# Kernel optimization log

Measured on AMD Instinct MI355X. Metric: run time of the kernel, lower is better.

## Reference

```python
import jax, jax.numpy as jnp
import numpy as np

jax.config.update("jax_enable_x64", True)

N = 3
NX = (N ** 2) ** 3          # 729 decision vars (flattened 9x9x9 one-hot board)
M2 = 128                    # dense inequality rows (G2)
QPEN = 0.1                  # Qpenalty -> Q = QPEN * I
NITER = 10                  # fixed interior-point iterations
SIGMA = 0.1                 # centering parameter
B = 16                      # batch of puzzles


def setup_inputs() -> dict:
    key = jax.random.key(0)
    k1, k2 = jax.random.split(key)
    puzzles = jax.random.uniform(k1, (B, 9, 9, 9), dtype=jnp.float32)
    G2 = jax.random.uniform(k2, (M2, NX), minval=-1.0, maxval=1.0, dtype=jnp.float32)
    z2 = jnp.zeros((NX,), jnp.float32)
    s2 = jnp.ones((M2,), jnp.float32)
    return {"puzzles": puzzles, "G2": G2, "z2": z2, "s2": s2}


def _qp_solve(p, G2, h):
    """Solve min 0.5 z'Qz + p'z  s.t. [-I; G2] z <= h for a batch of p.

    Primal-dual interior-point method, fixed NITER steps, exploiting the
    block structure G = [-I; G2]:  G' D G = diag(d1) + G2' D2 G2.
    p: (B, NX) float64. Returns z: (B, NX).
    """
    Bn, nx = p.shape
    G = jnp.concatenate([-jnp.eye(nx, dtype=p.dtype), G2], axis=0)  # (m, nx)
    m = G.shape[0]
    eye = jnp.eye(nx, dtype=p.dtype)

    z0 = jnp.zeros((Bn, nx), p.dtype)
    s0 = jnp.ones((Bn, m), p.dtype)
    lam0 = jnp.ones((Bn, m), p.dtype)

    def maxstep(x, dx):
        # largest alpha<=1 keeping x + alpha*dx > 0 (fraction-to-boundary 0.99)
        ratio = jnp.where(dx < 0, -x / jnp.where(dx < 0, dx, -1.0), jnp.inf)
        return jnp.minimum(1.0, 0.99 * jnp.min(ratio, axis=1))

    def step(carry, _):
        z, s, lam = carry
        Gz = z @ G.T                                   # (B, m)
        rd = QPEN * z + p + lam @ G                    # dual residual (B, nx)
        rp = Gz + s - h                                # primal residual (B, m)
        mu = jnp.mean(s * lam, axis=1, keepdims=True)  # (B, 1)
        d = lam / s                                    # (B, m)
        v = SIGMA * mu / s - lam + d * rp              # (B, m)
        rhs = -(rd + v @ G)                            # (B, nx)
        # K = Q + G' D G = diag(QPEN + d1) + G2' D2 G2  (block-sparse structure)
        K = jnp.einsum('mi,bm,mj->bij', G2, d[:, nx:], G2)
        K = K + eye[None] * (QPEN + d[:, :nx])[:, :, None]
        dz = jnp.linalg.solve(K, rhs[..., None])[..., 0]
        Gdz = dz @ G.T
        ds = -rp - Gdz
        dlam = v + d * Gdz
        alpha = jnp.minimum(maxstep(s, ds), maxstep(lam, dlam))[:, None]
        return (z + alpha * dz, s + alpha * ds, lam + alpha * dlam), None

    (z, _, _), _ = jax.lax.scan(step, (z0, s0, lam0), None, length=NITER)
    return z


def reference(puzzles, G2, z2, s2):
    Bn = puzzles.shape[0]
    G2d = G2.astype(jnp.float64)
    z2d = z2.astype(jnp.float64)
    s2d = s2.astype(jnp.float64)
    p = -puzzles.reshape(Bn, -1).astype(jnp.float64)     # (B, NX)
    h2 = G2d @ z2d + s2d                                 # (M2,)
    h = jnp.concatenate([jnp.zeros(NX, jnp.float64), h2])
    z = _qp_solve(p, G2d, h)
    return z.astype(jnp.float32).reshape(puzzles.shape)
```

## Files before the change

### kernel.cpp

```cpp
#include <hip/hip_runtime.h>
#include <math.h>

#define NXQ 729
#define M2Q 128
#define MQ  857
#define BQ  16
#define QPEN_ 0.1
#define SIGMA_ 0.1

typedef double d4 __attribute__((ext_vector_type(4)));

constexpr int OFF_P    = 0;
constexpr int OFF_H2   = OFF_P + BQ*NXQ;
constexpr int OFF_Q2   = OFF_H2 + M2Q;
constexpr int OFF_TP   = OFF_Q2 + BQ*M2Q;
constexpr int ST_Z    = 0;
constexpr int ST_S    = 729;
constexpr int ST_LAM  = 1586;
constexpr int ST_RP   = 2443;
constexpr int ST_V    = 3300;
constexpr int ST_AINV = 4157;
constexpr int ST_Y    = 4886;
constexpr int ST_GZ   = 5615;
constexpr int STB     = 5743;
constexpr int OFF_ST  = OFF_TP + 12*BQ*M2Q;
constexpr int OFF_SG  = OFF_ST + 2*BQ*STB;

constexpr int L_SL   = 0;
constexpr int L_US   = 16512;
constexpr int L_INVD = 16640;
constexpr int L_RED2 = 16768;
constexpr int SH_FUSED = (16768 + 544) * 8;
constexpr int D_DZ   = 0;
constexpr int D_RED  = 736;
constexpr int D_SC   = 744;
constexpr int D_Q2   = 752;
constexpr int D_YL   = 880;
constexpr int D_SN   = 944;
constexpr int D_LN   = 1801;
constexpr int D_PART = 2658;
constexpr int D_AINV = 12672;
constexpr int AR_W   = 3168;
constexpr int SH_PS  = 12672 * 8;

__device__ __constant__ int TRI_R[10] = {0,1,1,2,2,2,3,3,3,3};
__device__ __constant__ int TRI_C[10] = {0,0,1,0,1,2,0,1,2,3};
__device__ __constant__ int TRL_R[28] = {0,1,1,2,2,2,3,3,3,3,4,4,4,4,4,5,5,5,5,5,5,6,6,6,6,6,6,6};
__device__ __constant__ int TRL_C[28] = {0,0,1,0,1,2,0,1,2,3,0,1,2,3,4,0,1,2,3,4,5,0,1,2,3,4,5,6};

__device__ __forceinline__ double wred_sum(double v) {
#pragma unroll
  for (int off = 32; off > 0; off >>= 1) v += __shfl_down(v, off, 64);
  return v;
}
__device__ __forceinline__ double wred_min(double v) {
#pragma unroll
  for (int off = 32; off > 0; off >>= 1) v = fmin(v, __shfl_down(v, off, 64));
  return v;
}
__device__ __forceinline__ double rsqrt64(double x) {
  double r = (double)rsqrtf((float)x);
  r = r * (1.5 - 0.5 * x * r * r);
  r = r * (1.5 - 0.5 * x * r * r);
  return r;
}

__global__ __launch_bounds__(512)
void init_kernel(const float* __restrict__ puzzles, const float* __restrict__ G2,
                 const float* __restrict__ z2in, const float* __restrict__ s2in,
                 double* __restrict__ ws) {
  const int blk = blockIdx.x;
  const int tid = threadIdx.x, wave = tid >> 6, lane = tid & 63;
  __shared__ double sm[32];
  if (blk < BQ) {
    const int bb = blk;
    double* st = ws + OFF_ST + bb * STB;
    for (int i = tid; i < NXQ; i += 512) {
      ws[OFF_P + bb * NXQ + i] = -(double)puzzles[bb * NXQ + i];
      st[ST_Z + i] = 0.0;
      st[ST_AINV + i] = 1.0 / (QPEN_ + 1.0);
      st[ST_RP + i] = 1.0;
      st[ST_V + i] = SIGMA_;
    }
    for (int i = tid; i < MQ; i += 512) { st[ST_S + i] = 1.0; st[ST_LAM + i] = 1.0; }
    if (tid < M2Q) st[ST_GZ + tid] = 0.0;
  } else {
    const int r = blk - 16;
    double acc = 0.0;
    for (int kx = tid; kx < NXQ; kx += 512)
      acc += (double)G2[r * NXQ + kx] * (double)z2in[kx];
    acc = wred_sum(acc);
    if (lane == 0) sm[wave] = acc;
    __syncthreads();
    if (tid == 0) {
      double t = 0.0;
#pragma unroll
      for (int w = 0; w < 8; ++w) t += sm[w];
      const double h2r = t + (double)s2in[r];
      ws[OFF_H2 + r] = h2r;
      sm[16] = h2r;
    }
    __syncthreads();
    if (tid < BQ) {
      double* st = ws + OFF_ST + tid * STB;
      const double rp2 = 1.0 - sm[16];
      st[ST_RP + NXQ + r] = rp2;
      st[ST_V  + NXQ + r] = rp2 - 0.9;
      ws[OFF_Q2 + tid * M2Q + r] = rp2 + 0.1;
    }
  }
}

__device__ __forceinline__ void sbuild_core(const float* __restrict__ G2,
                                            const double* __restrict__ ainv,
                                            double* __restrict__ arena,
                                            double* __restrict__ Sgb, const int tile) {
  const int tid = threadIdx.x, wave = tid >> 6, lane = tid & 63;
  const int R0 = TRI_R[tile] * 32, C0 = TRI_C[tile] * 32;
  double* As = arena + wave * AR_W;
  double* Bs = As + 1584;
  const int k0w = wave * 183;
  const int kend = min(k0w + 183, NXQ);
  const int rg4 = (lane >> 3) * 4, cg4 = (lane & 7) * 4;
  const int kk16 = lane & 15, rsub = lane >> 4;
  double acc[4][4];
#pragma unroll
  for (int i = 0; i < 4; ++i)
#pragma unroll
    for (int j = 0; j < 4; ++j) acc[i][j] = 0.0;
  float pa[24], pb[24];
  if (wave < 4) {
#pragma unroll
    for (int it = 0; it < 24; ++it) {
      const int kk = (it >> 3) * 16 + kk16;
      const int rr = (it & 7) * 4 + rsub;
      const int k = k0w + kk;
      const int kc = (k < kend) ? k : (kend - 1);
      pa[it] = G2[(R0 + rr) * NXQ + kc];
      pb[it] = G2[(C0 + rr) * NXQ + kc];
    }
  }
  for (int ch = 0; ch < 4; ++ch) {
    __syncthreads();
    if (wave < 4) {
#pragma unroll
      for (int it = 0; it < 24; ++it) {
        const int kk = (it >> 3) * 16 + kk16;
        const int rr = (it & 7) * 4 + rsub;
        const int k = k0w + ch * 48 + kk;
        const bool ok = (k < kend);
        const double aik = ok ? ainv[k] : 0.0;
        const double av = ok ? (double)pa[it] * aik : 0.0;
        const double bv = ok ? (double)pb[it] : 0.0;
        As[kk * 33 + rr] = av;
        Bs[kk * 33 + rr] = bv;
      }
      if (ch < 3) {
#pragma unroll
        for (int it = 0; it < 24; ++it) {
          const int kk = (it >> 3) * 16 + kk16;
          const int rr = (it & 7) * 4 + rsub;
          const int k = k0w + (ch + 1) * 48 + kk;
          const int kc = (k < kend) ? k : (kend - 1);
          pa[it] = G2[(R0 + rr) * NXQ + kc];
          pb[it] = G2[(C0 + rr) * NXQ + kc];
        }
      }
    }
    __syncthreads();
    if (wave < 4) {
#pragma unroll 8
      for (int q = 0; q < 48; ++q) {
        const double a0 = As[q*33 + rg4 + 0], a1 = As[q*33 + rg4 + 1],
                     a2 = As[q*33 + rg4 + 2], a3 = As[q*33 + rg4 + 3];
        const double b0 = Bs[q*33 + cg4 + 0], b1 = Bs[q*33 + cg4 + 1],
                     b2 = Bs[q*33 + cg4 + 2], b3 = Bs[q*33 + cg4 + 3];
        acc[0][0] += a0*b0; acc[0][1] += a0*b1; acc[0][2] += a0*b2; acc[0][3] += a0*b3;
        acc[1][0] += a1*b0; acc[1][1] += a1*b1; acc[1][2] += a1*b2; acc[1][3] += a1*b3;
        acc[2][0] += a2*b0; acc[2][1] += a2*b1; acc[2][2] += a2*b2; acc[2][3] += a2*b3;
        acc[3][0] += a3*b0; acc[3][1] += a3*b1; acc[3][2] += a3*b2; acc[3][3] += a3*b3;
      }
    }
  }
  __syncthreads();
  if (wave < 4) {
#pragma unroll
    for (int i = 0; i < 4; ++i)
#pragma unroll
      for (int j = 0; j < 4; ++j)
        As[(rg4 + i) * 33 + cg4 + j] = acc[i][j];
  }
  __syncthreads();
  for (int idx = tid; idx < 1024; idx += 512) {
    const int r = idx >> 5, c = idx & 31;
    const int o = r * 33 + c;
    const double v = arena[o] + arena[AR_W + o] + arena[2*AR_W + o] + arena[3*AR_W + o];
    Sgb[tile * 1024 + idx] = v;
  }
}

__global__ __launch_bounds__(512)
void ps_kernel(const float* __restrict__ G2, double* __restrict__ ws) {
  const int b = blockIdx.x, tile = blockIdx.y;
  const int tid = threadIdx.x, lane = tid & 63;
  extern __shared__ double sm[];
  double* st = ws + OFF_ST + b * STB;
  {
    double* uvec = sm;
    double* part = sm + 128;
    double* yl   = sm + 640;
    const int c0 = tile * 64;
    if (tid < M2Q) uvec[tid] = ws[OFF_Q2 + b * M2Q + tid];
    __syncthreads();
    const int kk = tid & 63, rq = tid >> 6;
    const int k = c0 + kk;
    const int kg = (k < NXQ) ? k : (NXQ - 1);
    {
      const float* gp = G2 + (rq * 16) * NXQ + kg;
      double acc = 0.0;
#pragma unroll
      for (int j = 0; j < 16; ++j) acc = fma((double)gp[j * NXQ], uvec[rq * 16 + j], acc);
      part[rq * 64 + kk] = acc;
    }
    __syncthreads();
    if (tid < 64) {
      const int k2 = c0 + tid;
      double y = 0.0;
      if (k2 < NXQ) {
        double w = 0.0;
#pragma unroll
        for (int q = 0; q < 8; ++q) w += part[q * 64 + tid];
        const double rhsk = -(QPEN_ * st[ST_Z + k2] + ws[OFF_P + b * NXQ + k2]
                              - st[ST_LAM + k2] - st[ST_V + k2] + w);
        y = st[ST_AINV + k2] * rhsk;
        st[ST_Y + k2] = y;
      }
      yl[tid] = y;
    }
    __syncthreads();
    {
      const double yv = yl[lane];
      double pp[16];
#pragma unroll
      for (int jr = 0; jr < 16; ++jr)
        pp[jr] = (double)G2[((tid >> 6) * 16 + jr) * NXQ + kg] * yv;
#pragma unroll
      for (int st2 = 0; st2 < 4; ++st2) {
        const int m = 32 >> st2, half = 8 >> st2;
        const bool hi = (lane & m) != 0;
#pragma unroll
        for (int r = 0; r < 8; ++r) {
          if (r < half) {
            const double send = hi ? pp[r] : pp[r + half];
            const double recv = __shfl_xor(send, m, 64);
            pp[r] = (hi ? pp[r + half] : pp[r]) + recv;
          }
        }
      }
      double tot = pp[0];
      tot += __shfl_xor(tot, 2, 64);
      tot += __shfl_xor(tot, 1, 64);
      if ((lane & 3) == 0)
        ws[OFF_TP + (tile * BQ + b) * M2Q + (tid >> 6) * 16 + ((lane >> 2) & 15)] = tot;
    }
    __syncthreads();
  }
  if (tile < 10)
    sbuild_core(G2, st + ST_AINV, sm, ws + OFF_SG + b * 10240, tile);
}

__global__ __launch_bounds__(512, 1)
void dps_kernel(const float* __restrict__ G2, double* __restrict__ ws,
                float* __restrict__ out, const int ph, const int last) {
  const int b = blockIdx.x, chunk = blockIdx.y;
  const int tid = threadIdx.x, wave = tid >> 6, lane = tid & 63;
  extern __shared__ double sm[];
  double (*Sl)[129] = (double(*)[129])(sm + L_SL);
  double* us   = sm + L_US;
  double* invd = sm + L_INVD;
  double* red2 = sm + L_RED2;
  const double* R = ws + OFF_ST + ph * BQ * STB + b * STB;
  double*       W = ws + OFF_ST + (1 - ph) * BQ * STB + b * STB;
  double* Sgb  = ws + OFF_SG + b * 10240;
  const int c0 = chunk * 64;

#pragma unroll
  for (int t = 0; t < 10; ++t) {
    const int R0 = TRI_R[t] * 32, C0 = TRI_C[t] * 32;
    for (int e = tid; e < 1024; e += 512) {
      const int r = e >> 5, c = e & 31;
      Sl[R0 + r][C0 + c] = Sgb[t * 1024 + e];
    }
  }
  if (tid < M2Q) {
    double t = 0.0;
#pragma unroll
    for (int c = 0; c < 12; ++c) t += ws[OFF_TP + (c * BQ + b) * M2Q + tid];
    us[tid] = t;
  }
  __syncthreads();
  if (tid < M2Q) Sl[tid][tid] += R[ST_S + NXQ + tid] / R[ST_LAM + NXQ + tid];
  __syncthreads();

  int rowm[4], colm[4];
  {
    const int rc = lane & 15, kq = lane >> 4;
    const double avr = (kq == 0) ? (double)rc : 0.0;
    const double bv1 = (kq == 0) ? 1.0 : 0.0;
    const double av1 = (kq == 0) ? 1.0 : 0.0;
    const double bvc = (kq == 0) ? (double)rc : 0.0;
    d4 zero = {0.0, 0.0, 0.0, 0.0};
    d4 dr = __builtin_amdgcn_mfma_f64_16x16x4f64(avr, bv1, zero, 0, 0, 0);
    d4 dc = __builtin_amdgcn_mfma_f64_16x16x4f64(av1, bvc, zero, 0, 0, 0);
#pragma unroll
    for (int e = 0; e < 4; ++e) { rowm[e] = (int)dr[e]; colm[e] = (int)dc[e]; }
  }
  const int rc16 = lane & 15, kq4 = lane >> 4;

  auto panel16 = [&](const int K0) {
    const int r = lane;
    double a[16];
#pragma unroll
    for (int c = 0; c < 16; ++c) a[c] = Sl[K0 + r][K0 + c];
#pragma unroll
    for (int c = 0; c < 16; ++c) {
      const double dcc = __shfl(a[c], c, 64);
      const double rs = rsqrt64(dcc);
      a[c] *= rs;
      if (lane == c) invd[K0 + c] = rs;
#pragma unroll
      for (int k2 = c + 1; k2 < 16; ++k2) {
        const double lkc = __shfl(a[c], k2, 64);
        a[k2] = fma(-a[c], lkc, a[k2]);
      }
    }
#pragma unroll
    for (int c = 0; c < 16; ++c) Sl[K0 + r][K0 + c] = a[c];
  };

  auto tile_upd = [&](const int K0, const int i0, const int j0) {
    d4 tacc;
#pragma unroll
    for (int e = 0; e < 4; ++e) tacc[e] = Sl[i0 + rowm[e]][j0 + colm[e]];
#pragma unroll
    for (int m = 0; m < 4; ++m) {
      const double av = -Sl[i0 + rc16][K0 + 4 * m + kq4];
      const double bv =  Sl[j0 + rc16][K0 + 4 * m + kq4];
      tacc = __builtin_amdgcn_mfma_f64_16x16x4f64(av, bv, tacc, 0, 0, 0);
    }
#pragma unroll
    for (int e = 0; e < 4; ++e) Sl[i0 + rowm[e]][j0 + colm[e]] = tacc[e];
  };

  if (wave == 0 && lane < 16) panel16(0);
  __syncthreads();

  for (int kb = 0; kb < 8; ++kb) {
    const int K0 = kb * 16, J0 = K0 + 16, T = 128 - J0;
    if (tid <= T) {
      const bool isU = (tid == T);
      double l[16];
      if (isU) {
#pragma unroll
        for (int c = 0; c < 16; ++c) l[c] = us[K0 + c];
      } else {
#pragma unroll
        for (int c = 0; c < 16; ++c) l[c] = Sl[J0 + tid][K0 + c];
      }
#pragma unroll
      for (int c = 0; c < 16; ++c) {
        const double lc = l[c] * invd[K0 + c];
        l[c] = lc;
#pragma unroll
        for (int k2 = c + 1; k2 < 16; ++k2)
          l[k2] = fma(-lc, Sl[K0 + k2][K0 + c], l[k2]);
      }
      if (isU) {
#pragma unroll
        for (int c = 0; c < 16; ++c) us[K0 + c] = l[c];
      } else {
#pragma unroll
        for (int c = 0; c < 16; ++c) Sl[J0 + tid][K0 + c] = l[c];
      }
    }
    __syncthreads();

    if (kb < 7) {
      if (tid < T) {
        double acc = 0.0;
#pragma unroll
        for (int c = 0; c < 16; ++c) acc = fma(Sl[J0 + tid][K0 + c], us[K0 + c], acc);
        us[J0 + tid] -= acc;
      }
      if (wave == 7) tile_upd(K0, J0, J0);
      __syncthreads();
      const int Tb = 7 - kb;
      const int nt = (Tb * (Tb + 1)) >> 1;
      if (wave == 0) {
        if (lane < 16) panel16(J0);
      } else {
        for (int idx = wave; idx < nt; idx += 7)
          tile_upd(K0, J0 + TRL_R[idx] * 16, J0 + TRL_C[idx] * 16);
      }
      __syncthreads();
    }
  }

  for (int kb = 7; kb >= 0; --kb) {
    const int K0 = kb * 16;
    if (kb < 7) {
      const int c = tid & 15, ch = tid >> 4;
      double part = 0.0;
      for (int k = K0 + 16 + ch; k < 128; k += 32) part = fma(Sl[k][K0 + c], us[k], part);
      red2[ch * 17 + c] = part;
    }
    __syncthreads();
    if (wave == 0 && lane < 16) {
      const int j = lane;
      double x = us[K0 + j];
      if (kb < 7) {
        double acc = 0.0;
#pragma unroll
        for (int q = 0; q < 32; ++q) acc += red2[q * 17 + j];
        x -= acc;
      }
      double colv[16];
#pragma unroll
      for (int c = 0; c < 16; ++c) colv[c] = Sl[K0 + c][K0 + j];
      const double iv = invd[K0 + j];
#pragma unroll
      for (int cc = 0; cc < 16; ++cc) {
        const int c = 15 - cc;
        const double xiv = x * iv;
        const double uc = __shfl(xiv, c, 64);
        if (j == c) x = xiv;
        else if (j < c) x = fma(-colv[c], uc, x);
      }
      us[K0 + j] = x;
    }
    __syncthreads();
  }
  if (tid < M2Q) invd[tid] = (R[ST_S + NXQ + tid] / R[ST_LAM + NXQ + tid]) * us[tid];
  __syncthreads();
  double* g2b = invd;

  double* dzl   = sm + D_DZ;
  double* red   = sm + D_RED;
  double* sc    = sm + D_SC;
  double* ainvn = sm + D_AINV;
  double* q2l   = sm + D_Q2;
  double* yl    = sm + D_YL;
  double* snew  = sm + D_SN;
  double* lnew  = sm + D_LN;
  double* part  = sm + D_PART;

  for (int k = tid; k < NXQ; k += 512) {
    double acc = 0.0;
    const float* gp = G2 + k;
#pragma unroll 16
    for (int r = 0; r < M2Q; ++r) acc = fma((double)gp[r * NXQ], us[r], acc);
    dzl[k] = R[ST_Y + k] - R[ST_AINV + k] * acc;
  }
  __syncthreads();

  double lmin = 1e300;
  for (int i = tid; i < MQ; i += 512) {
    const double si = R[ST_S + i], li = R[ST_LAM + i], di = li / si;
    double dsi, dlami;
    if (i < NXQ) {
      const double dz = dzl[i];
      dsi = dz - R[ST_RP + i];
      dlami = R[ST_V + i] - di * dz;
    } else {
      const double g = g2b[i - NXQ];
      dsi = -R[ST_RP + i] - g;
      dlami = R[ST_V + i] + di * g;
    }
    snew[i] = dsi; lnew[i] = dlami;
    if (dsi < 0.0)   lmin = fmin(lmin, -si / dsi);
    if (dlami < 0.0) lmin = fmin(lmin, -li / dlami);
  }
  lmin = wred_min(lmin);
  if (lane == 0) red[wave] = lmin;
  __syncthreads();
  if (tid == 0) {
    double m = red[0];
#pragma unroll
    for (int w = 1; w < 8; ++w) m = fmin(m, red[w]);
    sc[0] = fmin(1.0, 0.99 * m);
  }
  __syncthreads();
  const double alpha = sc[0];

  if (last) {
    const int k2 = c0 + (tid & 63);
    if (tid < 64 && k2 < NXQ)
      out[b * NXQ + k2] = (float)(R[ST_Z + k2] + alpha * dzl[k2]);
    return;
  }

  double musum = 0.0;
  for (int i = tid; i < MQ; i += 512) {
    const double si = R[ST_S + i], li = R[ST_LAM + i];
    const double sn = si + alpha * snew[i], ln = li + alpha * lnew[i];
    snew[i] = sn; lnew[i] = ln;
    musum += sn * ln;
  }
  musum = wred_sum(musum);
  if (lane == 0) red[wave] = musum;
  __syncthreads();
  if (tid == 0) {
    double t = 0.0;
#pragma unroll
    for (int w = 0; w < 8; ++w) t += red[w];
    sc[1] = SIGMA_ * (t / (double)MQ);
  }
  __syncthreads();
  const double smu = sc[1];

  for (int i = tid; i < MQ; i += 512) {
    const double sn = snew[i], ln = lnew[i], di = ln / sn;
    if (i < NXQ) {
      const double zn = R[ST_Z + i] + alpha * dzl[i];
      const double rpn = sn - zn;
      const double vn = smu / sn - ln + di * rpn;
      const double an = 1.0 / (QPEN_ + di);
      ainvn[i] = an;
      if ((i >> 6) == chunk) {
        W[ST_Z + i] = zn; W[ST_S + i] = sn; W[ST_LAM + i] = ln;
        W[ST_RP + i] = rpn; W[ST_V + i] = vn; W[ST_AINV + i] = an;
      }
    } else {
      const int m = i - NXQ;
      const double gzn = R[ST_GZ + m] + alpha * g2b[m];
      const double rpn = gzn + sn - ws[OFF_H2 + m];
      const double vn = smu / sn - ln + di * rpn;
      q2l[m] = ln + vn;
      if (chunk == 0) {
        W[ST_S + i] = sn; W[ST_LAM + i] = ln;
        W[ST_RP + i] = rpn; W[ST_V + i] = vn; W[ST_GZ + m] = gzn;
      }
    }
  }
  __syncthreads();

  {
    const int kk = tid & 63, rq = tid >> 6;
    const int k = c0 + kk;
    const int kg = (k < NXQ) ? k : (NXQ - 1);
    {
      const float* gp = G2 + (rq * 16) * NXQ + kg;
      double acc = 0.0;
#pragma unroll
      for (int j = 0; j < 16; ++j) acc = fma((double)gp[j * NXQ], q2l[rq * 16 + j], acc);
      part[rq * 64 + kk] = acc;
    }
    __syncthreads();
    if (tid < 64) {
      const int k2 = c0 + tid;
      double y = 0.0;
      if (k2 < NXQ) {
        double w = 0.0;
#pragma unroll
        for (int q = 0; q < 8; ++q) w += part[q * 64 + tid];
        const double sn = snew[k2], ln = lnew[k2], di = ln / sn;
        const double zn = R[ST_Z + k2] + alpha * dzl[k2];
        const double rpn = sn - zn;
        const double vn = smu / sn - ln + di * rpn;
        const double rhsk = -(QPEN_ * zn + ws[OFF_P + b * NXQ + k2] - ln - vn + w);
        y = ainvn[k2] * rhsk;
        W[ST_Y + k2] = y;
      }
      yl[tid] = y;
    }
    __syncthreads();
    {
      const double yv = yl[lane];
      double pp[16];
#pragma unroll
      for (int jr = 0; jr < 16; ++jr)
        pp[jr] = (double)G2[((tid >> 6) * 16 + jr) * NXQ + kg] * yv;
#pragma unroll
      for (int st2 = 0; st2 < 4; ++st2) {
        const int m = 32 >> st2, half = 8 >> st2;
        const bool hi = (lane & m) != 0;
#pragma unroll
        for (int r = 0; r < 8; ++r) {
          if (r < half) {
            const double send = hi ? pp[r] : pp[r + half];
            const double recv = __shfl_xor(send, m, 64);
            pp[r] = (hi ? pp[r + half] : pp[r]) + recv;
          }
        }
      }
      double tot = pp[0];
      tot += __shfl_xor(tot, 2, 64);
      tot += __shfl_xor(tot, 1, 64);
      if ((lane & 3) == 0)
        ws[OFF_TP + (chunk * BQ + b) * M2Q + (tid >> 6) * 16 + ((lane >> 2) & 15)] = tot;
    }
    __syncthreads();
  }

  if (chunk < 10)
    sbuild_core(G2, ainvn, sm, Sgb, chunk);
}

extern "C" void kernel_launch(void* const* d_in, const int* in_sizes, int n_in,
                              void* d_out, int out_size, void* d_ws, size_t ws_size,
                              hipStream_t stream) {
  const float* puzzles = (const float*)d_in[0];
  const float* G2      = (const float*)d_in[1];
  const float* z2      = (const float*)d_in[2];
  const float* s2      = (const float*)d_in[3];
  float* out = (float*)d_out;
  double* ws = (double*)d_ws;

  (void)hipFuncSetAttribute(reinterpret_cast<const void*>(&dps_kernel),
                            hipFuncAttributeMaxDynamicSharedMemorySize, SH_FUSED);
  (void)hipFuncSetAttribute(reinterpret_cast<const void*>(&ps_kernel),
                            hipFuncAttributeMaxDynamicSharedMemorySize, SH_PS);

  init_kernel<<<dim3(16 + M2Q), dim3(512), 0, stream>>>(puzzles, G2, z2, s2, ws);
  ps_kernel<<<dim3(BQ, 12), dim3(512), SH_PS, stream>>>(G2, ws);
  for (int it = 0; it < 10; ++it) {
    const int ph = it & 1;
    dps_kernel<<<dim3(BQ, 12), dim3(512), SH_FUSED, stream>>>(G2, ws, out, ph, (it == 9) ? 1 : 0);
  }
}
```

Baseline: 970.5 us.

## Split S-build tiles into K-halves computed with FP64 MFMA across more blocks

The G2'DG2 tile build now uses FP64 MFMA 16x16x4 instructions instead of scalar FMA outer products. Each tile's K range is split into two halves written as separate partial buffers, which the consumer sums on load. The grid grows from 12 to 16 blocks per batch so more CUs share the S-build work. The dz computation is also fused with the step-length ratio loop, removing one barrier. The cost is a larger workspace, extra partial-sum reads, and more blocks per launch.

```diff
diff --git a/kernel.cpp b/kernel.cpp
--- a/kernel.cpp
+++ b/kernel.cpp
@@ -24,6 +24,7 @@
 constexpr int ST_GZ   = 5615;
 constexpr int STB     = 5743;
 constexpr int OFF_ST  = OFF_TP + 12*BQ*M2Q;
+constexpr int SGB_B   = 20480;
 constexpr int OFF_SG  = OFF_ST + 2*BQ*STB;
 
 constexpr int L_SL   = 0;
@@ -65,6 +66,20 @@
   return r;
 }
 
+__device__ __forceinline__ void mfma_cdmap(int* rowm, int* colm) {
+  const int lane = threadIdx.x & 63;
+  const int rc = lane & 15, kq = lane >> 4;
+  const double avr = (kq == 0) ? (double)rc : 0.0;
+  const double bv1 = (kq == 0) ? 1.0 : 0.0;
+  const double av1 = (kq == 0) ? 1.0 : 0.0;
+  const double bvc = (kq == 0) ? (double)rc : 0.0;
+  d4 zero = {0.0, 0.0, 0.0, 0.0};
+  d4 dr = __builtin_amdgcn_mfma_f64_16x16x4f64(avr, bv1, zero, 0, 0, 0);
+  d4 dc = __builtin_amdgcn_mfma_f64_16x16x4f64(av1, bvc, zero, 0, 0, 0);
+#pragma unroll
+  for (int e = 0; e < 4; ++e) { rowm[e] = (int)dr[e]; colm[e] = (int)dc[e]; }
+}
+
 __global__ __launch_bounds__(512)
 void init_kernel(const float* __restrict__ puzzles, const float* __restrict__ G2,
                  const float* __restrict__ z2in, const float* __restrict__ s2in,
@@ -111,57 +126,53 @@
   }
 }
 
-__device__ __forceinline__ void sbuild_core(const float* __restrict__ G2,
+__device__ __forceinline__ void sbuild_half(const float* __restrict__ G2,
                                             const double* __restrict__ ainv,
                                             double* __restrict__ arena,
-                                            double* __restrict__ Sgb, const int tile) {
+                                            double* __restrict__ Sgb,
+                                            const int tile, const int half,
+                                            const int* rowm, const int* colm) {
   const int tid = threadIdx.x, wave = tid >> 6, lane = tid & 63;
   const int R0 = TRI_R[tile] * 32, C0 = TRI_C[tile] * 32;
   double* As = arena + wave * AR_W;
   double* Bs = As + 1584;
-  const int k0w = wave * 183;
-  const int kend = min(k0w + 183, NXQ);
-  const int rg4 = (lane >> 3) * 4, cg4 = (lane & 7) * 4;
+  const int kw0 = half * 368 + wave * 92;
+  const int kwend = min(kw0 + 92, NXQ);
   const int kk16 = lane & 15, rsub = lane >> 4;
-  double acc[4][4];
-#pragma unroll
-  for (int i = 0; i < 4; ++i)
-#pragma unroll
-    for (int j = 0; j < 4; ++j) acc[i][j] = 0.0;
+  const int rc = lane & 15, kq = lane >> 4;
+  d4 c00 = {0.0, 0.0, 0.0, 0.0}, c01 = c00, c10 = c00, c11 = c00;
   float pa[24], pb[24];
   if (wave < 4) {
 #pragma unroll
     for (int it = 0; it < 24; ++it) {
       const int kk = (it >> 3) * 16 + kk16;
       const int rr = (it & 7) * 4 + rsub;
-      const int k = k0w + kk;
-      const int kc = (k < kend) ? k : (kend - 1);
+      const int k = kw0 + kk;
+      const int kc = (k < kwend) ? k : (kwend - 1);
       pa[it] = G2[(R0 + rr) * NXQ + kc];
       pb[it] = G2[(C0 + rr) * NXQ + kc];
     }
   }
-  for (int ch = 0; ch < 4; ++ch) {
+  for (int ch = 0; ch < 2; ++ch) {
     __syncthreads();
     if (wave < 4) {
 #pragma unroll
       for (int it = 0; it < 24; ++it) {
         const int kk = (it >> 3) * 16 + kk16;
         const int rr = (it & 7) * 4 + rsub;
-        const int k = k0w + ch * 48 + kk;
-        const bool ok = (k < kend);
+        const int k = kw0 + ch * 48 + kk;
+        const bool ok = (k < kwend);
         const double aik = ok ? ainv[k] : 0.0;
-        const double av = ok ? (double)pa[it] * aik : 0.0;
-        const double bv = ok ? (double)pb[it] : 0.0;
-        As[kk * 33 + rr] = av;
-        Bs[kk * 33 + rr] = bv;
-      }
-      if (ch < 3) {
+        As[kk * 33 + rr] = ok ? (double)pa[it] * aik : 0.0;
+        Bs[kk * 33 + rr] = ok ? (double)pb[it] : 0.0;
+      }
+      if (ch == 0) {
 #pragma unroll
         for (int it = 0; it < 24; ++it) {
           const int kk = (it >> 3) * 16 + kk16;
           const int rr = (it & 7) * 4 + rsub;
-          const int k = k0w + (ch + 1) * 48 + kk;
-          const int kc = (k < kend) ? k : (kend - 1);
+          const int k = kw0 + 48 + kk;
+          const int kc = (k < kwend) ? k : (kwend - 1);
           pa[it] = G2[(R0 + rr) * NXQ + kc];
           pb[it] = G2[(C0 + rr) * NXQ + kc];
         }
@@ -169,33 +180,49 @@
     }
     __syncthreads();
     if (wave < 4) {
-#pragma unroll 8
-      for (int q = 0; q < 48; ++q) {
-        const double a0 = As[q*33 + rg4 + 0], a1 = As[q*33 + rg4 + 1],
-                     a2 = As[q*33 + rg4 + 2], a3 = As[q*33 + rg4 + 3];
-        const double b0 = Bs[q*33 + cg4 + 0], b1 = Bs[q*33 + cg4 + 1],
-                     b2 = Bs[q*33 + cg4 + 2], b3 = Bs[q*33 + cg4 + 3];
-        acc[0][0] += a0*b0; acc[0][1] += a0*b1; acc[0][2] += a0*b2; acc[0][3] += a0*b3;
-        acc[1][0] += a1*b0; acc[1][1] += a1*b1; acc[1][2] += a1*b2; acc[1][3] += a1*b3;
-        acc[2][0] += a2*b0; acc[2][1] += a2*b1; acc[2][2] += a2*b2; acc[2][3] += a2*b3;
-        acc[3][0] += a3*b0; acc[3][1] += a3*b1; acc[3][2] += a3*b2; acc[3][3] += a3*b3;
+#pragma unroll
+      for (int s = 0; s < 12; ++s) {
+        const int ko = (s * 4 + kq) * 33;
+        const double a0 = As[ko + rc],      a1 = As[ko + 16 + rc];
+        const double b0 = Bs[ko + rc],      b1 = Bs[ko + 16 + rc];
+        c00 = __builtin_amdgcn_mfma_f64_16x16x4f64(a0, b0, c00, 0, 0, 0);
+        c01 = __builtin_amdgcn_mfma_f64_16x16x4f64(a0, b1, c01, 0, 0, 0);
+        c10 = __builtin_amdgcn_mfma_f64_16x16x4f64(a1, b0, c10, 0, 0, 0);
+        c11 = __builtin_amdgcn_mfma_f64_16x16x4f64(a1, b1, c11, 0, 0, 0);
       }
     }
   }
   __syncthreads();
   if (wave < 4) {
 #pragma unroll
-    for (int i = 0; i < 4; ++i)
-#pragma unroll
-      for (int j = 0; j < 4; ++j)
-        As[(rg4 + i) * 33 + cg4 + j] = acc[i][j];
+    for (int e = 0; e < 4; ++e) {
+      As[rowm[e] * 33 + colm[e]]              = c00[e];
+      As[rowm[e] * 33 + 16 + colm[e]]         = c01[e];
+      As[(16 + rowm[e]) * 33 + colm[e]]       = c10[e];
+      As[(16 + rowm[e]) * 33 + 16 + colm[e]]  = c11[e];
+    }
   }
   __syncthreads();
   for (int idx = tid; idx < 1024; idx += 512) {
     const int r = idx >> 5, c = idx & 31;
     const int o = r * 33 + c;
     const double v = arena[o] + arena[AR_W + o] + arena[2*AR_W + o] + arena[3*AR_W + o];
-    Sgb[tile * 1024 + idx] = v;
+    Sgb[(tile * 2 + half) * 1024 + idx] = v;
+  }
+}
+
+__device__ __forceinline__ void run_sbuild_units(const float* __restrict__ G2,
+                                                 const double* __restrict__ ainv,
+                                                 double* __restrict__ arena,
+                                                 double* __restrict__ Sgb,
+                                                 const int y,
+                                                 const int* rowm, const int* colm) {
+  if (y < 12) {
+    sbuild_half(G2, ainv, arena, Sgb, y >> 1, y & 1, rowm, colm);
+  } else {
+    const int u0 = 12 + (y - 12) * 2;
+    sbuild_half(G2, ainv, arena, Sgb, u0 >> 1, u0 & 1, rowm, colm);
+    sbuild_half(G2, ainv, arena, Sgb, (u0 + 1) >> 1, (u0 + 1) & 1, rowm, colm);
   }
 }
 
@@ -205,7 +232,7 @@
   const int tid = threadIdx.x, lane = tid & 63;
   extern __shared__ double sm[];
   double* st = ws + OFF_ST + b * STB;
-  {
+  if (tile < 12) {
     double* uvec = sm;
     double* part = sm + 128;
     double* yl   = sm + 640;
@@ -265,8 +292,12 @@
     }
     __syncthreads();
   }
-  if (tile < 10)
-    sbuild_core(G2, st + ST_AINV, sm, ws + OFF_SG + b * 10240, tile);
+  {
+    int rowm[4], colm[4];
+    mfma_cdmap(rowm, colm);
+    run_sbuild_units(G2, st + ST_AINV, sm, ws + OFF_SG + b * SGB_B, tile,
+                     rowm, colm);
+  }
 }
 
 __global__ __launch_bounds__(512, 1)
@@ -281,7 +312,7 @@
   double* red2 = sm + L_RED2;
   const double* R = ws + OFF_ST + ph * BQ * STB + b * STB;
   double*       W = ws + OFF_ST + (1 - ph) * BQ * STB + b * STB;
-  double* Sgb  = ws + OFF_SG + b * 10240;
+  double* Sgb  = ws + OFF_SG + b * SGB_B;
   const int c0 = chunk * 64;
 
 #pragma unroll
@@ -289,7 +320,7 @@
     const int R0 = TRI_R[t] * 32, C0 = TRI_C[t] * 32;
     for (int e = tid; e < 1024; e += 512) {
       const int r = e >> 5, c = e & 31;
-      Sl[R0 + r][C0 + c] = Sgb[t * 1024 + e];
+      Sl[R0 + r][C0 + c] = Sgb[(t * 2) * 1024 + e] + Sgb[(t * 2 + 1) * 1024 + e];
     }
   }
   if (tid < M2Q) {
@@ -303,18 +334,7 @@
   __syncthreads();
 
   int rowm[4], colm[4];
-  {
-    const int rc = lane & 15, kq = lane >> 4;
-    const double avr = (kq == 0) ? (double)rc : 0.0;
-    const double bv1 = (kq == 0) ? 1.0 : 0.0;
-    const double av1 = (kq == 0) ? 1.0 : 0.0;
-    const double bvc = (kq == 0) ? (double)rc : 0.0;
-    d4 zero = {0.0, 0.0, 0.0, 0.0};
-    d4 dr = __builtin_amdgcn_mfma_f64_16x16x4f64(avr, bv1, zero, 0, 0, 0);
-    d4 dc = __builtin_amdgcn_mfma_f64_16x16x4f64(av1, bvc, zero, 0, 0, 0);
-#pragma unroll
-    for (int e = 0; e < 4; ++e) { rowm[e] = (int)dr[e]; colm[e] = (int)dc[e]; }
-  }
+  mfma_cdmap(rowm, colm);
   const int rc16 = lane & 15, kq4 = lane >> 4;
 
   auto panel16 = [&](const int K0) {
@@ -454,28 +474,27 @@
   double* lnew  = sm + D_LN;
   double* part  = sm + D_PART;
 
+  double lmin = 1e300;
   for (int k = tid; k < NXQ; k += 512) {
-    double acc = 0.0;
+    double accv = 0.0;
     const float* gp = G2 + k;
 #pragma unroll 16
-    for (int r = 0; r < M2Q; ++r) acc = fma((double)gp[r * NXQ], us[r], acc);
-    dzl[k] = R[ST_Y + k] - R[ST_AINV + k] * acc;
-  }
-  __syncthreads();
-
-  double lmin = 1e300;
-  for (int i = tid; i < MQ; i += 512) {
+    for (int r = 0; r < M2Q; ++r) accv = fma((double)gp[r * NXQ], us[r], accv);
+    const double dzv = R[ST_Y + k] - R[ST_AINV + k] * accv;
+    dzl[k] = dzv;
+    const double si = R[ST_S + k], li = R[ST_LAM + k], di = li / si;
+    const double dsi = dzv - R[ST_RP + k];
+    const double dlami = R[ST_V + k] - di * dzv;
+    snew[k] = dsi; lnew[k] = dlami;
+    if (dsi < 0.0)   lmin = fmin(lmin, -si / dsi);
+    if (dlami < 0.0) lmin = fmin(lmin, -li / dlami);
+  }
+  if (tid < M2Q) {
+    const int i = NXQ + tid;
     const double si = R[ST_S + i], li = R[ST_LAM + i], di = li / si;
-    double dsi, dlami;
-    if (i < NXQ) {
-      const double dz = dzl[i];
-      dsi = dz - R[ST_RP + i];
-      dlami = R[ST_V + i] - di * dz;
-    } else {
-      const double g = g2b[i - NXQ];
-      dsi = -R[ST_RP + i] - g;
-      dlami = R[ST_V + i] + di * g;
-    }
+    const double g = g2b[tid];
+    const double dsi = -R[ST_RP + i] - g;
+    const double dlami = R[ST_V + i] + di * g;
     snew[i] = dsi; lnew[i] = dlami;
     if (dsi < 0.0)   lmin = fmin(lmin, -si / dsi);
     if (dlami < 0.0) lmin = fmin(lmin, -li / dlami);
@@ -544,7 +563,7 @@
   }
   __syncthreads();
 
-  {
+  if (chunk < 12) {
     const int kk = tid & 63, rq = tid >> 6;
     const int k = c0 + kk;
     const int kg = (k < NXQ) ? k : (NXQ - 1);
@@ -602,8 +621,7 @@
     __syncthreads();
   }
 
-  if (chunk < 10)
-    sbuild_core(G2, ainvn, sm, Sgb, chunk);
+  run_sbuild_units(G2, ainvn, sm, Sgb, chunk, rowm, colm);
 }
 
 extern "C" void kernel_launch(void* const* d_in, const int* in_sizes, int n_in,
@@ -622,9 +640,9 @@
                             hipFuncAttributeMaxDynamicSharedMemorySize, SH_PS);
 
   init_kernel<<<dim3(16 + M2Q), dim3(512), 0, stream>>>(puzzles, G2, z2, s2, ws);
-  ps_kernel<<<dim3(BQ, 12), dim3(512), SH_PS, stream>>>(G2, ws);
+  ps_kernel<<<dim3(BQ, 16), dim3(512), SH_PS, stream>>>(G2, ws);
   for (int it = 0; it < 10; ++it) {
     const int ph = it & 1;
-    dps_kernel<<<dim3(BQ, 12), dim3(512), SH_FUSED, stream>>>(G2, ws, out, ph, (it == 9) ? 1 : 0);
-  }
-}
+    dps_kernel<<<dim3(BQ, 16), dim3(512), SH_FUSED, stream>>>(G2, ws, out, ph, (it == 9) ? 1 : 0);
+  }
+}
```

New measurement: 829.5 us. -14.5%, faster.
